# Kernel optimization log

Measured on AMD Instinct MI355X. Metric: run time of the kernel, lower is better.

Reference implementation:

```python
import jax, jax.numpy as jnp
import numpy as np
import math


def _rel_pos_tables(W):
    # continuous relative coords table: [(2W-1), (2W-1), 2]
    c = np.arange(-(W - 1), W, dtype=np.float32)
    table = np.stack(np.meshgrid(c, c, indexing='ij'), axis=-1)  # [2W-1,2W-1,2]
    table = table / (W - 1)
    table = table * 8.0
    table = np.sign(table) * np.log2(np.abs(table) + 1.0) / math.log2(8.0)
    # relative position index: [W*W, W*W]
    coords = np.stack(np.meshgrid(np.arange(W), np.arange(W), indexing='ij'))  # [2,W,W]
    flat = coords.reshape(2, -1)  # [2, W*W]
    rel = flat[:, :, None] - flat[:, None, :]  # [2, N, N]
    rel = rel.transpose(1, 2, 0).copy()
    rel[:, :, 0] += W - 1
    rel[:, :, 1] += W - 1
    rel[:, :, 0] *= 2 * W - 1
    idx = rel.sum(-1)  # [N, N]
    return jnp.asarray(table), jnp.asarray(idx, dtype=jnp.int32)


def setup_inputs() -> dict:
    key = jax.random.key(0)
    ks = jax.random.split(key, 10)
    dim, W, H = 512, 8, 16
    N = W * W
    B_, nW = 2048, 256
    s = 0.02
    inp = {
        'x': jax.random.normal(ks[0], (B_, N, dim), jnp.float32),
        'mask': jax.random.normal(ks[1], (nW, N, N), jnp.float32),
        'qkv_w': jax.random.normal(ks[2], (dim, 3 * dim), jnp.float32) * s,
        'qkv_b': jnp.zeros((3 * dim,), jnp.float32),
        'logit_scale': jnp.full((H, 1, 1), math.log(10.0), jnp.float32),
        'cpb_w1': jax.random.normal(ks[3], (2, 512), jnp.float32) * s,
        'cpb_b1': jnp.zeros((512,), jnp.float32),
        'cpb_w2': jax.random.normal(ks[4], (512, H), jnp.float32) * s,
        'proj_w': jax.random.normal(ks[5], (dim, dim), jnp.float32) * s,
        'proj_b': jnp.zeros((dim,), jnp.float32),
        'window_size': W,
        'num_heads': H,
    }
    return inp


def reference(x, mask, qkv_w, qkv_b, logit_scale, cpb_w1, cpb_b1, cpb_w2,
              proj_w, proj_b, window_size, num_heads):
    B_, N, C = x.shape
    H = num_heads
    hd = C // H

    qkv = (x @ qkv_w + qkv_b).reshape(B_, N, 3, H, hd)
    qkv = jnp.transpose(qkv, (2, 0, 3, 1, 4))  # [3, B_, H, N, hd]
    q, k, v = qkv[0], qkv[1], qkv[2]

    # cosine attention: L2-normalize q, k (eps matches F.normalize)
    q = q / jnp.clip(jnp.linalg.norm(q, axis=-1, keepdims=True), 1e-12)
    k = k / jnp.clip(jnp.linalg.norm(k, axis=-1, keepdims=True), 1e-12)

    attn = jnp.einsum('bhnd,bhmd->bhnm', q, k)
    scale = jnp.exp(jnp.minimum(logit_scale, math.log(1.0 / 0.01)))  # [H,1,1]
    attn = attn * scale[None]

    # continuous relative position bias
    table, idx = _rel_pos_tables(window_size)
    t = jax.nn.relu(table @ cpb_w1 + cpb_b1) @ cpb_w2  # [2W-1, 2W-1, H]
    t = t.reshape(-1, H)
    bias = t[idx.reshape(-1)].reshape(N, N, H)
    bias = 16.0 * jax.nn.sigmoid(jnp.transpose(bias, (2, 0, 1)))  # [H, N, N]
    attn = attn + bias[None]

    # mask add: [nW, N, N]
    nW = mask.shape[0]
    attn = attn.reshape(B_ // nW, nW, H, N, N) + mask[None, :, None]
    attn = attn.reshape(B_, H, N, N)

    attn = jax.nn.softmax(attn, axis=-1)
    out = jnp.einsum('bhnm,bhmd->bhnd', attn, v)
    out = jnp.transpose(out, (0, 2, 1, 3)).reshape(B_, N, C)
    out = out @ proj_w + proj_b
    return out
```

## Files before the change

kernel.cpp:

```cpp
#include <hip/hip_runtime.h>
#include <hip/hip_bf16.h>
#include <stdint.h>

typedef __attribute__((ext_vector_type(8))) short short8;
typedef __attribute__((ext_vector_type(8))) _Float16 half8;
typedef __attribute__((ext_vector_type(4))) float f32x4;

#define HSTR ((size_t)131072 * 32)

__device__ __forceinline__ unsigned short f2h(float f) {
  union { _Float16 h; unsigned short u; } c;
  c.h = (_Float16)f;
  return c.u;
}
__device__ __forceinline__ float h2f(unsigned short u) {
  union { _Float16 h; unsigned short u; } c;
  c.u = u;
  return (float)c.h;
}
__device__ __forceinline__ void gload_lds16(const void* g, void* l) {
  __builtin_amdgcn_global_load_lds(
      (const __attribute__((address_space(1))) unsigned int*)g,
      (__attribute__((address_space(3))) unsigned int*)l, 16, 0, 0);
}


__global__ __launch_bounds__(256) void cast_f16(const float* __restrict__ in,
                                                unsigned short* __restrict__ out) {
  const size_t total = (size_t)131072 * 512 / 8;
  size_t stride = (size_t)gridDim.x * 256;
  for (size_t i = blockIdx.x * 256 + threadIdx.x; i < total; i += stride) {
    f32x4 f0 = *(const f32x4*)(in + i * 8);
    f32x4 f1 = *(const f32x4*)(in + i * 8 + 4);
    short8 o;
#pragma unroll
    for (int e = 0; e < 4; e++) {
      o[e] = (short)f2h(f0[e]);
      o[4 + e] = (short)f2h(f1[e]);
    }
    *(short8*)(out + i * 8) = o;
  }
}

__global__ __launch_bounds__(256) void transpose_cast(const float* __restrict__ in,
                                                      unsigned short* __restrict__ out,
                                                      int K, int N) {
  __shared__ float tile[32][33];
  int nb = N / 32;
  int bx = blockIdx.x % nb, by = blockIdx.x / nb;
  int tx = threadIdx.x & 31, ty = threadIdx.x >> 5;
#pragma unroll
  for (int r = 0; r < 32; r += 8)
    tile[ty + r][tx] = in[(size_t)(by * 32 + ty + r) * N + bx * 32 + tx];
  __syncthreads();
#pragma unroll
  for (int r = 0; r < 32; r += 8)
    out[(size_t)(bx * 32 + ty + r) * K + by * 32 + tx] = f2h(tile[tx][ty + r]);
}

__device__ __forceinline__ float cpb_coord(int a) {
  float v = (float)(a - 7) * (8.0f / 7.0f);
  float s = (v > 0.f) ? 1.f : ((v < 0.f) ? -1.f : 0.f);
  return s * log2f(fabsf(v) + 1.f) * (1.f / 3.f);
}

__global__ __launch_bounds__(64) void cpb_mlp(const float* __restrict__ w1,
                                              const float* __restrict__ b1,
                                              const float* __restrict__ w2,
                                              float* __restrict__ t_out) {
  int e = blockIdx.x;
  int dy = e / 15, dx = e % 15;
  float in0 = cpb_coord(dy), in1 = cpb_coord(dx);
  float acc[16];
#pragma unroll
  for (int o = 0; o < 16; ++o) acc[o] = 0.f;
  for (int u = threadIdx.x; u < 512; u += 64) {
    float hsum = fmaxf(in0 * w1[u] + in1 * w1[512 + u] + b1[u], 0.f);
#pragma unroll
    for (int o = 0; o < 16; ++o) acc[o] += hsum * w2[u * 16 + o];
  }
#pragma unroll
  for (int o = 0; o < 16; ++o) {
    float v = acc[o];
    v += __shfl_xor(v, 1);  v += __shfl_xor(v, 2);  v += __shfl_xor(v, 4);
    v += __shfl_xor(v, 8);  v += __shfl_xor(v, 16); v += __shfl_xor(v, 32);
    acc[o] = v;
  }
  if (threadIdx.x == 0)
#pragma unroll
    for (int o = 0; o < 16; ++o) t_out[e * 16 + o] = acc[o];
}

__global__ __launch_bounds__(256) void bias_kernel(const float* __restrict__ t,
                                                   float* __restrict__ bias) {
  int idx = blockIdx.x * 256 + threadIdx.x;
  int j = idx & 63, i = (idx >> 6) & 63, h = idx >> 12;
  int dy = (i >> 3) - (j >> 3) + 7;
  int dx = (i & 7) - (j & 7) + 7;
  float v = t[(dy * 15 + dx) * 16 + h];
  bias[idx] = 16.f / (1.f + expf(-v));
}

__global__ __launch_bounds__(512, 1) void qkv_gemm(const unsigned short* __restrict__ xh,
                                                   const unsigned short* __restrict__ Wt,
                                                   const float* __restrict__ bvec,
                                                   unsigned short* __restrict__ qout,
                                                   unsigned short* __restrict__ kout,
                                                   unsigned short* __restrict__ vout) {
  __shared__ __align__(16) short smem[49152];
  const int bid = (blockIdx.x & 7) * 384 + (blockIdx.x >> 3);
  const int nt = bid % 6;
  const int mt = bid / 6;
  const int m0 = mt * 256, n0 = nt * 256;
  const int t = threadIdx.x;
  const int l = t & 63, wid = t >> 6;
  const int wm = wid >> 2, wn = wid & 3;
  const int fr = l & 15, fg = l >> 4;

  f32x4 acc[8][4];
#pragma unroll
  for (int i = 0; i < 8; i++)
#pragma unroll
    for (int j = 0; j < 4; j++) acc[i][j] = f32x4{0.f, 0.f, 0.f, 0.f};

  auto STAGE = [&](int bsel, int kt) {
#pragma unroll
    for (int it = 0; it < 2; ++it) {
      int flat = it * 512 + t;
      int row = flat >> 2, s = flat & 3;
      int g = s ^ (row & 3);
      gload_lds16(xh + (size_t)(m0 + row) * 512 + kt * 32 + g * 8,
                  &smem[bsel * 8192 + flat * 8]);
      gload_lds16(Wt + (size_t)(n0 + row) * 512 + kt * 32 + g * 8,
                  &smem[24576 + bsel * 8192 + flat * 8]);
    }
  };

  STAGE(0, 0);
  STAGE(1, 1);
  __builtin_amdgcn_sched_barrier(0);

  for (int kt = 0; kt < 16; ++kt) {
    const int cur = kt % 3;
    if (kt < 14) STAGE((kt + 2) % 3, kt + 2);
    __builtin_amdgcn_sched_barrier(0);
    if (kt < 14)       asm volatile("s_waitcnt vmcnt(8)" ::: "memory");
    else if (kt == 14) asm volatile("s_waitcnt vmcnt(4)" ::: "memory");
    else               asm volatile("s_waitcnt vmcnt(0)" ::: "memory");
    __builtin_amdgcn_sched_barrier(0);
    __builtin_amdgcn_s_barrier();
    __builtin_amdgcn_sched_barrier(0);
    {
      const short* Ab = &smem[cur * 8192];
      const short* Bb = &smem[24576 + cur * 8192];
      half8 bfr[4];
#pragma unroll
      for (int j = 0; j < 4; ++j) {
        int row = wn * 64 + j * 16 + fr;
        bfr[j] = *(const half8*)&Bb[row * 32 + ((fg ^ (row & 3)) << 3)];
      }
#pragma unroll
      for (int i = 0; i < 8; ++i) {
        int rowA = wm * 128 + i * 16 + fr;
        half8 a0 = *(const half8*)&Ab[rowA * 32 + ((fg ^ (rowA & 3)) << 3)];
#pragma unroll
        for (int j = 0; j < 4; ++j)
          acc[i][j] = __builtin_amdgcn_mfma_f32_16x16x32_f16(a0, bfr[j], acc[i][j], 0, 0, 0);
      }
    }
    __builtin_amdgcn_sched_barrier(0);
    __builtin_amdgcn_s_barrier();
    __builtin_amdgcn_sched_barrier(0);
  }

  unsigned short* dst;
  int g0;
  if (nt < 2)      { dst = qout; g0 = nt * 8; }
  else if (nt < 4) { dst = kout; g0 = (nt - 2) * 8; }
  else             { dst = vout; g0 = (nt - 4) * 8; }
#pragma unroll
  for (int hh = 0; hh < 2; ++hh) {
    if (hh) __syncthreads();
    if (wm == hh) {
#pragma unroll
      for (int i = 0; i < 8; ++i)
#pragma unroll
        for (int j = 0; j < 4; ++j) {
          int col = wn * 64 + j * 16 + fr;
          float bb = bvec[n0 + col];
#pragma unroll
          for (int r = 0; r < 4; ++r)
            smem[(i * 16 + fg * 4 + r) * 256 + col] = (short)f2h(acc[i][j][r] + bb);
        }
    }
    __syncthreads();
#pragma unroll
    for (int it = 0; it < 8; ++it) {
      int flat = it * 512 + t;
      int row = flat >> 5, c32 = flat & 31;
      *(short8*)(dst + (size_t)(g0 + (c32 >> 2)) * HSTR +
                 (size_t)(m0 + hh * 128 + row) * 32 + (c32 & 3) * 8) =
          *(short8*)&smem[row * 256 + c32 * 8];
    }
  }
}

__global__ __launch_bounds__(256) void attn_kernel(const unsigned short* __restrict__ qws,
                                                   const unsigned short* __restrict__ kws,
                                                   const unsigned short* __restrict__ vws,
                                                   const float* __restrict__ bias,
                                                   const float* __restrict__ mask,
                                                   const float* __restrict__ logit_scale,
                                                   unsigned short* __restrict__ aout) {
  const int blk = (blockIdx.x & 7) * 4096 + (blockIdx.x >> 3);
  const int h = blk >> 11;
  const int b = blk & 2047;
  const int wmi = b & 255;
  const int t = threadIdx.x, l = t & 63, w = t >> 6;

  __shared__ __align__(16) short qs[64 * 32], ks[64 * 32];
  __shared__ __align__(16) short vt[32 * 72];
  __shared__ __align__(16) short plds[4 * 16 * 72];
  __shared__ float invs[64];

  const float scale = __expf(fminf(logit_scale[h], 4.6051702f));

  {
    const int r = t >> 2, c4 = t & 3;
    const size_t base = (size_t)h * HSTR + (size_t)(b * 64 + r) * 32 + c4 * 8;
    {
      uint4 raw = *(const uint4*)(qws + base);
      unsigned int rr[4] = {raw.x, raw.y, raw.z, raw.w};
      float f[8];
#pragma unroll
      for (int e = 0; e < 4; e++) {
        f[2 * e]     = h2f((unsigned short)(rr[e] & 0xffff));
        f[2 * e + 1] = h2f((unsigned short)(rr[e] >> 16));
      }
      float ss = 0.f;
#pragma unroll
      for (int e = 0; e < 8; e++) ss += f[e] * f[e];
      ss += __shfl_xor(ss, 1);
      ss += __shfl_xor(ss, 2);
      float inv = 1.f / fmaxf(sqrtf(ss), 1e-12f);
      short8 o;
#pragma unroll
      for (int e = 0; e < 8; e++) o[e] = (short)f2h(f[e] * inv);
      *(short8*)&qs[r * 32 + c4 * 8] = o;
    }
    {
      uint4 raw = *(const uint4*)(kws + base);
      unsigned int rr[4] = {raw.x, raw.y, raw.z, raw.w};
      float f[8];
#pragma unroll
      for (int e = 0; e < 4; e++) {
        f[2 * e]     = h2f((unsigned short)(rr[e] & 0xffff));
        f[2 * e + 1] = h2f((unsigned short)(rr[e] >> 16));
      }
      float ss = 0.f;
#pragma unroll
      for (int e = 0; e < 8; e++) ss += f[e] * f[e];
      ss += __shfl_xor(ss, 1);
      ss += __shfl_xor(ss, 2);
      float inv = 1.f / fmaxf(sqrtf(ss), 1e-12f);
      short8 o;
#pragma unroll
      for (int e = 0; e < 8; e++) o[e] = (short)f2h(f[e] * inv);
      *(short8*)&ks[r * 32 + c4 * 8] = o;
    }
    {
      uint4 raw = *(const uint4*)(vws + base);
      unsigned int rr[4] = {raw.x, raw.y, raw.z, raw.w};
#pragma unroll
      for (int e2 = 0; e2 < 4; e2++) {
        vt[(c4 * 8 + 2 * e2 + 0) * 72 + r] = (short)(rr[e2] & 0xffff);
        vt[(c4 * 8 + 2 * e2 + 1) * 72 + r] = (short)(rr[e2] >> 16);
      }
    }
  }
  __syncthreads();

  const int fr = l & 15, fg = l >> 4;
  half8 bq = *(half8*)&qs[(w * 16 + fr) * 32 + fg * 8];

  f32x4 st[4];
#pragma unroll
  for (int kt = 0; kt < 4; kt++) {
    half8 ak = *(half8*)&ks[(kt * 16 + fr) * 32 + fg * 8];
    st[kt] = __builtin_amdgcn_mfma_f32_16x16x32_f16(ak, bq, f32x4{0.f, 0.f, 0.f, 0.f}, 0, 0, 0);
  }
  const int q = w * 16 + fr;
  const int kbase = fg * 4;
  float sv[16];
  float mx = -1e30f;
#pragma unroll
  for (int kt = 0; kt < 4; kt++) {
    f32x4 b4 = *(const f32x4*)&bias[(size_t)(h * 64 + q) * 64 + kt * 16 + kbase];
    f32x4 m4 = *(const f32x4*)&mask[(size_t)(wmi * 64 + q) * 64 + kt * 16 + kbase];
#pragma unroll
    for (int j = 0; j < 4; j++) {
      float xv = st[kt][j] * scale + b4[j] + m4[j];
      sv[kt * 4 + j] = xv;
      mx = fmaxf(mx, xv);
    }
  }
  mx = fmaxf(mx, __shfl_xor(mx, 16));
  mx = fmaxf(mx, __shfl_xor(mx, 32));
  float sum = 0.f;
#pragma unroll
  for (int i2 = 0; i2 < 16; i2++) {
    float p = __expf(sv[i2] - mx);
    sv[i2] = p;
    sum += p;
  }
  sum += __shfl_xor(sum, 16);
  sum += __shfl_xor(sum, 32);

  short* pl = &plds[w * 16 * 72];
#pragma unroll
  for (int kt = 0; kt < 4; kt++)
#pragma unroll
    for (int j = 0; j < 4; j += 2) {
      unsigned int pack = (unsigned int)f2h(sv[kt * 4 + j]) |
                          ((unsigned int)f2h(sv[kt * 4 + j + 1]) << 16);
      *(unsigned int*)&pl[fr * 72 + kt * 16 + kbase + j] = pack;
    }
  if (fg == 0) invs[q] = 1.f / sum;
  __syncthreads();

  half8 pa0 = *(half8*)&pl[fr * 72 + fg * 8];
  half8 pa1 = *(half8*)&pl[fr * 72 + 32 + fg * 8];
#pragma unroll
  for (int nt2 = 0; nt2 < 2; nt2++) {
    half8 bv0 = *(half8*)&vt[(nt2 * 16 + fr) * 72 + fg * 8];
    half8 bv1 = *(half8*)&vt[(nt2 * 16 + fr) * 72 + 32 + fg * 8];
    f32x4 o = f32x4{0.f, 0.f, 0.f, 0.f};
    o = __builtin_amdgcn_mfma_f32_16x16x32_f16(pa0, bv0, o, 0, 0, 0);
    o = __builtin_amdgcn_mfma_f32_16x16x32_f16(pa1, bv1, o, 0, 0, 0);
    const int qo = w * 16 + fg * 4;
    const int hd = nt2 * 16 + fr;
#pragma unroll
    for (int r2 = 0; r2 < 4; r2++) {
      float vv = o[r2] * invs[qo + r2];
      qs[(qo + r2) * 32 + hd] = (short)f2h(vv);
    }
  }
  __syncthreads();
  {
    const int row = t >> 2, c = t & 3;
    *(short8*)(aout + (size_t)h * HSTR + (size_t)(b * 64 + row) * 32 + c * 8) =
        *(short8*)&qs[row * 32 + c * 8];
  }
}

__global__ __launch_bounds__(256) void proj_gemm(const unsigned short* __restrict__ A,
                                                 const unsigned short* __restrict__ Wt,
                                                 const float* __restrict__ bvec,
                                                 float* __restrict__ out) {
  __shared__ __align__(16) short smem[16384];
  const int bid = (blockIdx.x & 7) * 512 + (blockIdx.x >> 3);
  const int nt = bid & 3;
  const int mt = bid >> 2;
  const int m0 = mt * 128, n0 = nt * 128;
  const int t = threadIdx.x;
  const int l = t & 63, w = t >> 6;
  const int wm = w >> 1, wn = w & 1;
  const int fr = l & 15, fg = l >> 4;
  const int sch = t & 3;

  f32x4 acc[4][4];
#pragma unroll
  for (int i = 0; i < 4; i++)
#pragma unroll
    for (int j = 0; j < 4; j++) acc[i][j] = f32x4{0.f, 0.f, 0.f, 0.f};

  auto STAGE = [&](int bsel, int k0) {
#pragma unroll
    for (int it = 0; it < 2; ++it) {
      int flat = it * 256 + t;
      int row = flat >> 2;
      gload_lds16(A + (size_t)(k0 >> 5) * HSTR + (size_t)(m0 + row) * 32 + sch * 8,
                  &smem[bsel * 4096 + flat * 8]);
      gload_lds16(Wt + (size_t)(n0 + row) * 512 + k0 + sch * 8,
                  &smem[8192 + bsel * 4096 + flat * 8]);
    }
  };

  STAGE(0, 0);
  __syncthreads();
  int cur = 0;
  for (int k0 = 0; k0 < 512; k0 += 32) {
    if (k0 + 32 < 512) STAGE(cur ^ 1, k0 + 32);
    half8 af[4], bfr[4];
#pragma unroll
    for (int i = 0; i < 4; i++)
      af[i] = *(half8*)&smem[cur * 4096 + (wm * 64 + i * 16 + fr) * 32 + fg * 8];
#pragma unroll
    for (int j = 0; j < 4; j++)
      bfr[j] = *(half8*)&smem[8192 + cur * 4096 + (wn * 64 + j * 16 + fr) * 32 + fg * 8];
#pragma unroll
    for (int i = 0; i < 4; i++)
#pragma unroll
      for (int j = 0; j < 4; j++)
        acc[i][j] = __builtin_amdgcn_mfma_f32_16x16x32_f16(af[i], bfr[j], acc[i][j], 0, 0, 0);
    __syncthreads();
    cur ^= 1;
  }

  float* bounce = (float*)smem;
#pragma unroll
  for (int half = 0; half < 2; ++half) {
    if (wm == half) {
#pragma unroll
      for (int j = 0; j < 4; j++) {
        int col = wn * 64 + j * 16 + fr;
        float bb = bvec[n0 + col];
#pragma unroll
        for (int i = 0; i < 4; i++) {
          int row0 = i * 16 + fg * 4;
#pragma unroll
          for (int r = 0; r < 4; r++)
            bounce[(row0 + r) * 128 + col] = acc[i][j][r] + bb;
        }
      }
    }
    __syncthreads();
#pragma unroll
    for (int it = 0; it < 8; ++it) {
      int flat = it * 256 + t;
      int row = flat >> 5, c4 = flat & 31;
      *(f32x4*)(out + (size_t)(m0 + half * 64 + row) * 512 + n0 + c4 * 4) =
          *(f32x4*)&bounce[row * 128 + c4 * 4];
    }
    __syncthreads();
  }
}

extern "C" void kernel_launch(void* const* d_in, const int* in_sizes, int n_in,
                              void* d_out, int out_size, void* d_ws, size_t ws_size,
                              hipStream_t stream) {
  const float* x           = (const float*)d_in[0];
  const float* mask        = (const float*)d_in[1];
  const float* qkv_w       = (const float*)d_in[2];
  const float* qkv_b       = (const float*)d_in[3];
  const float* logit_scale = (const float*)d_in[4];
  const float* cpb_w1      = (const float*)d_in[5];
  const float* cpb_b1      = (const float*)d_in[6];
  const float* cpb_w2      = (const float*)d_in[7];
  const float* proj_w      = (const float*)d_in[8];
  const float* proj_b      = (const float*)d_in[9];
  (void)in_sizes; (void)n_in; (void)out_size; (void)ws_size;

  char* p = (char*)d_ws;
  unsigned short* Wqkv_t  = (unsigned short*)p; p += (size_t)1536 * 512 * 2;
  unsigned short* Wproj_t = (unsigned short*)p; p += (size_t)512 * 512 * 2;
  float* t_cpb            = (float*)p;          p += (size_t)225 * 16 * 4;
  float* biasb            = (float*)p;          p += (size_t)16 * 64 * 64 * 4;
  unsigned short* xh      = (unsigned short*)p; p += (size_t)131072 * 512 * 2;
  unsigned short* qbuf    = (unsigned short*)p; p += (size_t)131072 * 512 * 2;
  unsigned short* kbuf    = (unsigned short*)p; p += (size_t)131072 * 512 * 2;
  unsigned short* vbuf    = (unsigned short*)p; p += (size_t)131072 * 512 * 2;
  unsigned short* abuf    = (unsigned short*)p; p += (size_t)131072 * 512 * 2;

  cast_f16<<<2048, 256, 0, stream>>>(x, xh);
  transpose_cast<<<768, 256, 0, stream>>>(qkv_w, Wqkv_t, 512, 1536);
  transpose_cast<<<256, 256, 0, stream>>>(proj_w, Wproj_t, 512, 512);
  cpb_mlp<<<225, 64, 0, stream>>>(cpb_w1, cpb_b1, cpb_w2, t_cpb);
  bias_kernel<<<256, 256, 0, stream>>>(t_cpb, biasb);
  qkv_gemm<<<3072, 512, 0, stream>>>(xh, Wqkv_t, qkv_b, qbuf, kbuf, vbuf);
  attn_kernel<<<32768, 256, 0, stream>>>(qbuf, kbuf, vbuf, biasb, mask, logit_scale, abuf);
  proj_gemm<<<4096, 256, 0, stream>>>(abuf, Wproj_t, proj_b, (float*)d_out);
}
```

Baseline: 726.7 us.

## Restructure QKV GEMM into 8-phase ping-pong schedule with interleaved loads

Rewrites the QKV GEMM main loop from a triple-buffered single-K-tile pipeline into a double-buffered scheme. Each buffer holds two K tiles, and each iteration is split into 8 phases. In each phase the block issues one global-to-LDS load, reads a sub-block of fragments, and runs 8 MFMAs under raised wave priority, with barriers between phases. The goal is to interleave memory traffic with MFMA work more finely and hide load latency. In exchange it adds LDS usage (128KB), which limits occupancy, and many more barriers per iteration.

```diff
diff --git a/kernel.cpp b/kernel.cpp
--- a/kernel.cpp
+++ b/kernel.cpp
@@ -107,13 +107,13 @@
                                                    unsigned short* __restrict__ qout,
                                                    unsigned short* __restrict__ kout,
                                                    unsigned short* __restrict__ vout) {
-  __shared__ __align__(16) short smem[49152];
+  __shared__ __align__(16) short smem[65536];
   const int bid = (blockIdx.x & 7) * 384 + (blockIdx.x >> 3);
   const int nt = bid % 6;
   const int mt = bid / 6;
   const int m0 = mt * 256, n0 = nt * 256;
-  const int t = threadIdx.x;
-  const int l = t & 63, wid = t >> 6;
+  const int tid = threadIdx.x;
+  const int l = tid & 63, wid = tid >> 6;
   const int wm = wid >> 2, wn = wid & 3;
   const int fr = l & 15, fg = l >> 4;
 
@@ -123,54 +123,67 @@
 #pragma unroll
     for (int j = 0; j < 4; j++) acc[i][j] = f32x4{0.f, 0.f, 0.f, 0.f};
 
-  auto STAGE = [&](int bsel, int kt) {
-#pragma unroll
-    for (int it = 0; it < 2; ++it) {
-      int flat = it * 512 + t;
-      int row = flat >> 2, s = flat & 3;
-      int g = s ^ (row & 3);
-      gload_lds16(xh + (size_t)(m0 + row) * 512 + kt * 32 + g * 8,
-                  &smem[bsel * 8192 + flat * 8]);
-      gload_lds16(Wt + (size_t)(n0 + row) * 512 + kt * 32 + g * 8,
-                  &smem[24576 + bsel * 8192 + flat * 8]);
-    }
+  const int srow128 = tid >> 2, ss = tid & 3;
+  auto STAGE1 = [&](int db, int ktp, int tile, int p) {
+    int grow = (p & 1) * 128 + srow128;
+    int g = ss ^ (grow & 3);
+    if (((p >> 1) & 1) == 0)
+      gload_lds16(xh + (size_t)(m0 + grow) * 512 + tile * 32 + g * 8,
+                  &smem[db * 16384 + ktp * 8192 + grow * 32 + ss * 8]);
+    else
+      gload_lds16(Wt + (size_t)(n0 + grow) * 512 + tile * 32 + g * 8,
+                  &smem[32768 + db * 16384 + ktp * 8192 + grow * 32 + ss * 8]);
   };
 
-  STAGE(0, 0);
-  STAGE(1, 1);
+#pragma unroll
+  for (int p = 0; p < 8; ++p) STAGE1(0, p >> 2, p >> 2, p);
   __builtin_amdgcn_sched_barrier(0);
-
-  for (int kt = 0; kt < 16; ++kt) {
-    const int cur = kt % 3;
-    if (kt < 14) STAGE((kt + 2) % 3, kt + 2);
-    __builtin_amdgcn_sched_barrier(0);
-    if (kt < 14)       asm volatile("s_waitcnt vmcnt(8)" ::: "memory");
-    else if (kt == 14) asm volatile("s_waitcnt vmcnt(4)" ::: "memory");
-    else               asm volatile("s_waitcnt vmcnt(0)" ::: "memory");
-    __builtin_amdgcn_sched_barrier(0);
-    __builtin_amdgcn_s_barrier();
-    __builtin_amdgcn_sched_barrier(0);
-    {
-      const short* Ab = &smem[cur * 8192];
-      const short* Bb = &smem[24576 + cur * 8192];
-      half8 bfr[4];
-#pragma unroll
-      for (int j = 0; j < 4; ++j) {
-        int row = wn * 64 + j * 16 + fr;
-        bfr[j] = *(const half8*)&Bb[row * 32 + ((fg ^ (row & 3)) << 3)];
-      }
-#pragma unroll
-      for (int i = 0; i < 8; ++i) {
-        int rowA = wm * 128 + i * 16 + fr;
-        half8 a0 = *(const half8*)&Ab[rowA * 32 + ((fg ^ (rowA & 3)) << 3)];
-#pragma unroll
-        for (int j = 0; j < 4; ++j)
-          acc[i][j] = __builtin_amdgcn_mfma_f32_16x16x32_f16(a0, bfr[j], acc[i][j], 0, 0, 0);
-      }
-    }
-    __builtin_amdgcn_sched_barrier(0);
-    __builtin_amdgcn_s_barrier();
-    __builtin_amdgcn_sched_barrier(0);
+  asm volatile("s_waitcnt vmcnt(4)" ::: "memory");
+  __builtin_amdgcn_sched_barrier(0);
+  __builtin_amdgcn_s_barrier();
+  __builtin_amdgcn_sched_barrier(0);
+
+  for (int itr = 0; itr < 8; ++itr) {
+    const int cb = itr & 1;
+    const short* Ab = &smem[cb * 16384];
+    const short* Bb = &smem[32768 + cb * 16384];
+#pragma unroll
+    for (int p = 0; p < 8; ++p) {
+      const int ktp = p >> 2, q = p & 3;
+      const int i0 = (q & 1) * 4, j0 = (q >> 1) * 2;
+      half8 af[4], bf[2];
+#pragma unroll
+      for (int i = 0; i < 4; ++i) {
+        int row = wm * 128 + (i0 + i) * 16 + fr;
+        af[i] = *(const half8*)&Ab[ktp * 8192 + row * 32 + ((fg ^ (row & 3)) << 3)];
+      }
+#pragma unroll
+      for (int j = 0; j < 2; ++j) {
+        int row = wn * 64 + (j0 + j) * 16 + fr;
+        bf[j] = *(const half8*)&Bb[ktp * 8192 + row * 32 + ((fg ^ (row & 3)) << 3)];
+      }
+      if (itr < 7) STAGE1(cb ^ 1, p >> 2, 2 * itr + 2 + (p >> 2), p);
+      __builtin_amdgcn_sched_barrier(0);
+      __builtin_amdgcn_s_barrier();
+      asm volatile("s_waitcnt lgkmcnt(0)" ::: "memory");
+      __builtin_amdgcn_sched_barrier(0);
+      __builtin_amdgcn_s_setprio(1);
+#pragma unroll
+      for (int i = 0; i < 4; ++i)
+#pragma unroll
+        for (int j = 0; j < 2; ++j)
+          acc[i0 + i][j0 + j] =
+              __builtin_amdgcn_mfma_f32_16x16x32_f16(af[i], bf[j], acc[i0 + i][j0 + j], 0, 0, 0);
+      __builtin_amdgcn_s_setprio(0);
+      __builtin_amdgcn_sched_barrier(0);
+      if (p == 3 || p == 7) {
+        if (itr < 7) asm volatile("s_waitcnt vmcnt(4)" ::: "memory");
+        else         asm volatile("s_waitcnt vmcnt(0)" ::: "memory");
+        __builtin_amdgcn_sched_barrier(0);
+      }
+      __builtin_amdgcn_s_barrier();
+      __builtin_amdgcn_sched_barrier(0);
+    }
   }
 
   unsigned short* dst;
@@ -196,7 +209,7 @@
     __syncthreads();
 #pragma unroll
     for (int it = 0; it < 8; ++it) {
-      int flat = it * 512 + t;
+      int flat = it * 512 + tid;
       int row = flat >> 5, c32 = flat & 31;
       *(short8*)(dst + (size_t)(g0 + (c32 >> 2)) * HSTR +
                  (size_t)(m0 + hh * 128 + row) * 32 + (c32 & 3) * 8) =
```

New measurement: 736.6 us. No clear change (+1.4%).

## Precombine bias and mask into per-head MFMA-fragment-ordered table

Applied to the files above, without the earlier changes.

Replaces the per-head bias table with a combined bias+mask table of shape [H, nW, 64, 64], stored in the order the attention kernel's MFMA output fragments consume it. The attention kernel then reads one contiguous 64-byte chunk per lane instead of two strided loads from the bias and mask arrays. The loads are also issued before the QK MFMAs so their latency is hidden. In exchange, a 64 MB table has to be written each call and read back, which adds memory traffic compared with the 16 MB mask plus a small bias.

```diff
diff --git a/kernel.cpp b/kernel.cpp
--- a/kernel.cpp
+++ b/kernel.cpp
@@ -91,14 +91,28 @@
     for (int o = 0; o < 16; ++o) t_out[e * 16 + o] = acc[o];
 }
 
-__global__ __launch_bounds__(256) void bias_kernel(const float* __restrict__ t,
-                                                   float* __restrict__ bias) {
-  int idx = blockIdx.x * 256 + threadIdx.x;
-  int j = idx & 63, i = (idx >> 6) & 63, h = idx >> 12;
-  int dy = (i >> 3) - (j >> 3) + 7;
-  int dx = (i & 7) - (j & 7) + 7;
-  float v = t[(dy * 15 + dx) * 16 + h];
-  bias[idx] = 16.f / (1.f + expf(-v));
+__global__ __launch_bounds__(256) void combine_kernel(const float* __restrict__ t,
+                                                      const float* __restrict__ mask,
+                                                      float* __restrict__ combined) {
+  size_t F = ((size_t)blockIdx.x * 256 + threadIdx.x) * 8;
+  int p0 = (int)(F & 63);
+  int i = (int)((F >> 6) & 63);
+  int wmi = (int)((F >> 12) & 255);
+  int h = (int)(F >> 20);
+  int iy = i >> 3, ix = i & 7;
+  float vals[8];
+#pragma unroll
+  for (int e = 0; e < 8; ++e) {
+    int p = p0 + e;
+    int kt = p & 3, j = (p >> 2) & 3, fgp = p >> 4;
+    int c = kt * 16 + fgp * 4 + j;
+    int dy = iy - (c >> 3) + 7;
+    int dx = ix - (c & 7) + 7;
+    float bv = 16.f / (1.f + expf(-t[(dy * 15 + dx) * 16 + h]));
+    vals[e] = bv + mask[((size_t)wmi * 64 + i) * 64 + c];
+  }
+  *(f32x4*)(combined + F) = f32x4{vals[0], vals[1], vals[2], vals[3]};
+  *(f32x4*)(combined + F + 4) = f32x4{vals[4], vals[5], vals[6], vals[7]};
 }
 
 __global__ __launch_bounds__(512, 1) void qkv_gemm(const unsigned short* __restrict__ xh,
@@ -208,8 +222,7 @@
 __global__ __launch_bounds__(256) void attn_kernel(const unsigned short* __restrict__ qws,
                                                    const unsigned short* __restrict__ kws,
                                                    const unsigned short* __restrict__ vws,
-                                                   const float* __restrict__ bias,
-                                                   const float* __restrict__ mask,
+                                                   const float* __restrict__ combined,
                                                    const float* __restrict__ logit_scale,
                                                    unsigned short* __restrict__ aout) {
   const int blk = (blockIdx.x & 7) * 4096 + (blockIdx.x >> 3);
@@ -281,7 +294,15 @@
   __syncthreads();
 
   const int fr = l & 15, fg = l >> 4;
-  half8 bq = *(half8*)&qs[(w * 16 + fr) * 32 + fg * 8];
+  const int q = w * 16 + fr;
+
+  const float* cmb = combined + (((size_t)h * 256 + wmi) * 64 + q) * 64 + fg * 16;
+  f32x4 c0 = *(const f32x4*)cmb;
+  f32x4 c1 = *(const f32x4*)(cmb + 4);
+  f32x4 c2 = *(const f32x4*)(cmb + 8);
+  f32x4 c3 = *(const f32x4*)(cmb + 12);
+
+  half8 bq = *(half8*)&qs[q * 32 + fg * 8];
 
   f32x4 st[4];
 #pragma unroll
@@ -289,17 +310,15 @@
     half8 ak = *(half8*)&ks[(kt * 16 + fr) * 32 + fg * 8];
     st[kt] = __builtin_amdgcn_mfma_f32_16x16x32_f16(ak, bq, f32x4{0.f, 0.f, 0.f, 0.f}, 0, 0, 0);
   }
-  const int q = w * 16 + fr;
   const int kbase = fg * 4;
   float sv[16];
   float mx = -1e30f;
 #pragma unroll
   for (int kt = 0; kt < 4; kt++) {
-    f32x4 b4 = *(const f32x4*)&bias[(size_t)(h * 64 + q) * 64 + kt * 16 + kbase];
-    f32x4 m4 = *(const f32x4*)&mask[(size_t)(wmi * 64 + q) * 64 + kt * 16 + kbase];
 #pragma unroll
     for (int j = 0; j < 4; j++) {
-      float xv = st[kt][j] * scale + b4[j] + m4[j];
+      float cj = (j == 0) ? c0[kt] : (j == 1) ? c1[kt] : (j == 2) ? c2[kt] : c3[kt];
+      float xv = st[kt][j] * scale + cj;
       sv[kt * 4 + j] = xv;
       mx = fmaxf(mx, xv);
     }
@@ -455,7 +474,7 @@
   unsigned short* Wqkv_t  = (unsigned short*)p; p += (size_t)1536 * 512 * 2;
   unsigned short* Wproj_t = (unsigned short*)p; p += (size_t)512 * 512 * 2;
   float* t_cpb            = (float*)p;          p += (size_t)225 * 16 * 4;
-  float* biasb            = (float*)p;          p += (size_t)16 * 64 * 64 * 4;
+  float* combined         = (float*)p;          p += (size_t)16 * 256 * 64 * 64 * 4;
   unsigned short* xh      = (unsigned short*)p; p += (size_t)131072 * 512 * 2;
   unsigned short* qbuf    = (unsigned short*)p; p += (size_t)131072 * 512 * 2;
   unsigned short* kbuf    = (unsigned short*)p; p += (size_t)131072 * 512 * 2;
@@ -466,8 +485,8 @@
   transpose_cast<<<768, 256, 0, stream>>>(qkv_w, Wqkv_t, 512, 1536);
   transpose_cast<<<256, 256, 0, stream>>>(proj_w, Wproj_t, 512, 512);
   cpb_mlp<<<225, 64, 0, stream>>>(cpb_w1, cpb_b1, cpb_w2, t_cpb);
-  bias_kernel<<<256, 256, 0, stream>>>(t_cpb, biasb);
+  combine_kernel<<<8192, 256, 0, stream>>>(t_cpb, mask, combined);
   qkv_gemm<<<3072, 512, 0, stream>>>(xh, Wqkv_t, qkv_b, qbuf, kbuf, vbuf);
-  attn_kernel<<<32768, 256, 0, stream>>>(qbuf, kbuf, vbuf, biasb, mask, logit_scale, abuf);
+  attn_kernel<<<32768, 256, 0, stream>>>(qbuf, kbuf, vbuf, combined, logit_scale, abuf);
   proj_gemm<<<4096, 256, 0, stream>>>(abuf, Wproj_t, proj_b, (float*)d_out);
 }
```

Result: slower. 745.0 us (+2.5%).

## Triple-buffer proj GEMM loads with swizzled LDS and explicit vmcnt waits

Applied to the files above, without the earlier changes.

Moves the projection GEMM from a double-buffered to a three-stage LDS pipeline, prefetching two k-tiles ahead. It uses explicit s_waitcnt vmcnt counts and raw barriers in place of __syncthreads so global-to-LDS loads can stay in flight across iterations. An XOR swizzle of the 16-byte chunks per row is added to cut LDS bank conflicts on fragment reads. In exchange LDS use per block grows by half, which can lower occupancy, and the hand-set vmcnt counts depend on the exact number of loads issued per stage.

```diff
diff --git a/kernel.cpp b/kernel.cpp
--- a/kernel.cpp
+++ b/kernel.cpp
@@ -357,7 +357,7 @@
                                                  const unsigned short* __restrict__ Wt,
                                                  const float* __restrict__ bvec,
                                                  float* __restrict__ out) {
-  __shared__ __align__(16) short smem[16384];
+  __shared__ __align__(16) short smem[24576];
   const int bid = (blockIdx.x & 7) * 512 + (blockIdx.x >> 3);
   const int nt = bid & 3;
   const int mt = bid >> 2;
@@ -366,7 +366,6 @@
   const int l = t & 63, w = t >> 6;
   const int wm = w >> 1, wn = w & 1;
   const int fr = l & 15, fg = l >> 4;
-  const int sch = t & 3;
 
   f32x4 acc[4][4];
 #pragma unroll
@@ -374,42 +373,60 @@
 #pragma unroll
     for (int j = 0; j < 4; j++) acc[i][j] = f32x4{0.f, 0.f, 0.f, 0.f};
 
-  auto STAGE = [&](int bsel, int k0) {
+  auto STAGE = [&](int bsel, int kt) {
 #pragma unroll
     for (int it = 0; it < 2; ++it) {
       int flat = it * 256 + t;
-      int row = flat >> 2;
-      gload_lds16(A + (size_t)(k0 >> 5) * HSTR + (size_t)(m0 + row) * 32 + sch * 8,
+      int row = flat >> 2, s = flat & 3;
+      int g = s ^ (row & 3);
+      gload_lds16(A + (size_t)kt * HSTR + (size_t)(m0 + row) * 32 + g * 8,
                   &smem[bsel * 4096 + flat * 8]);
-      gload_lds16(Wt + (size_t)(n0 + row) * 512 + k0 + sch * 8,
-                  &smem[8192 + bsel * 4096 + flat * 8]);
+      gload_lds16(Wt + (size_t)(n0 + row) * 512 + kt * 32 + g * 8,
+                  &smem[12288 + bsel * 4096 + flat * 8]);
     }
   };
 
   STAGE(0, 0);
-  __syncthreads();
-  int cur = 0;
-  for (int k0 = 0; k0 < 512; k0 += 32) {
-    if (k0 + 32 < 512) STAGE(cur ^ 1, k0 + 32);
-    half8 af[4], bfr[4];
-#pragma unroll
-    for (int i = 0; i < 4; i++)
-      af[i] = *(half8*)&smem[cur * 4096 + (wm * 64 + i * 16 + fr) * 32 + fg * 8];
-#pragma unroll
-    for (int j = 0; j < 4; j++)
-      bfr[j] = *(half8*)&smem[8192 + cur * 4096 + (wn * 64 + j * 16 + fr) * 32 + fg * 8];
-#pragma unroll
-    for (int i = 0; i < 4; i++)
-#pragma unroll
-      for (int j = 0; j < 4; j++)
-        acc[i][j] = __builtin_amdgcn_mfma_f32_16x16x32_f16(af[i], bfr[j], acc[i][j], 0, 0, 0);
-    __syncthreads();
-    cur ^= 1;
+  STAGE(1, 1);
+  __builtin_amdgcn_sched_barrier(0);
+
+  for (int kt = 0; kt < 16; ++kt) {
+    const int cur = kt % 3;
+    if (kt < 14) STAGE((kt + 2) % 3, kt + 2);
+    __builtin_amdgcn_sched_barrier(0);
+    if (kt < 14)       asm volatile("s_waitcnt vmcnt(8)" ::: "memory");
+    else if (kt == 14) asm volatile("s_waitcnt vmcnt(4)" ::: "memory");
+    else               asm volatile("s_waitcnt vmcnt(0)" ::: "memory");
+    __builtin_amdgcn_sched_barrier(0);
+    __builtin_amdgcn_s_barrier();
+    __builtin_amdgcn_sched_barrier(0);
+    {
+      const short* Ab = &smem[cur * 4096];
+      const short* Bb = &smem[12288 + cur * 4096];
+      half8 bfr[4];
+#pragma unroll
+      for (int j = 0; j < 4; ++j) {
+        int row = wn * 64 + j * 16 + fr;
+        bfr[j] = *(const half8*)&Bb[row * 32 + ((fg ^ (row & 3)) << 3)];
+      }
+#pragma unroll
+      for (int i = 0; i < 4; ++i) {
+        int rowA = wm * 64 + i * 16 + fr;
+        half8 a0 = *(const half8*)&Ab[rowA * 32 + ((fg ^ (rowA & 3)) << 3)];
+#pragma unroll
+        for (int j = 0; j < 4; ++j)
+          acc[i][j] = __builtin_amdgcn_mfma_f32_16x16x32_f16(a0, bfr[j], acc[i][j], 0, 0, 0);
+      }
+    }
+    __builtin_amdgcn_sched_barrier(0);
+    __builtin_amdgcn_s_barrier();
+    __builtin_amdgcn_sched_barrier(0);
   }
 
   float* bounce = (float*)smem;
 #pragma unroll
   for (int half = 0; half < 2; ++half) {
+    if (half) __syncthreads();
     if (wm == half) {
 #pragma unroll
       for (int j = 0; j < 4; j++) {
```

New measurement: 714.5 us, median of 3. No clear change (-1.7%).
